# Optimization experiments

Measured on AMD Instinct MI355X. Metric: run time of the kernel, lower is better.

The kernel has to match this reference:

```python
import jax, jax.numpy as jnp
import numpy as np

N, E, IN_DIM, HID, PROJ, NG = 50000, 1600000, 128, 128, 128, 64


def setup_inputs() -> dict:
    key = jax.random.key(0)
    ks = jax.random.split(key, 12)
    def glorot(k, fan_in, fan_out):
        s = (6.0 / (fan_in + fan_out)) ** 0.5
        return jax.random.uniform(k, (fan_in, fan_out), jnp.float32, -s, s)
    x = jax.random.normal(ks[0], (N, IN_DIM), jnp.float32)
    edge_index = jax.random.randint(ks[1], (2, E), 0, N, jnp.int32)
    batch = jnp.sort(jax.random.randint(ks[2], (N,), 0, NG, jnp.int32))
    return {
        "x": x,
        "edge_index": edge_index,
        "batch": batch,
        "num_graphs": NG,
        "W1": glorot(ks[3], IN_DIM, HID), "b1": jnp.zeros((HID,), jnp.float32),
        "W2": glorot(ks[4], HID, HID),    "b2": jnp.zeros((HID,), jnp.float32),
        "pW1": glorot(ks[5], HID, HID),   "pb1": jnp.zeros((HID,), jnp.float32),
        "pW2": glorot(ks[6], HID, PROJ),  "pb2": jnp.zeros((PROJ,), jnp.float32),
    }


def _gcn_norm(edge_index, n_nodes):
    # add self loops, compute symmetric normalization (PyG GCNConv default)
    loop = jnp.arange(n_nodes, dtype=edge_index.dtype)
    src = jnp.concatenate([edge_index[0], loop])
    dst = jnp.concatenate([edge_index[1], loop])
    deg = jax.ops.segment_sum(jnp.ones_like(dst, jnp.float32), dst, num_segments=n_nodes)
    dinv = jnp.where(deg > 0, jax.lax.rsqrt(deg), 0.0)
    norm = dinv[src] * dinv[dst]  # [E+N]
    return src, dst, norm


def _gcn_conv(h, W, b, src, dst, norm, n_nodes):
    hw = h @ W                              # [N, out]
    msg = hw[src] * norm[:, None]           # gather + scale, [E+N, out]
    out = jax.ops.segment_sum(msg, dst, num_segments=n_nodes)  # scatter-add
    return out + b


def reference(x, edge_index, batch, num_graphs, W1, b1, W2, b2, pW1, pb1, pW2, pb2):
    n_nodes = x.shape[0]
    src, dst, norm = _gcn_norm(edge_index, n_nodes)
    # conv stack (dropout is identity in eval mode)
    h = jax.nn.relu(_gcn_conv(x, W1, b1, src, dst, norm, n_nodes))
    h = jax.nn.relu(_gcn_conv(h, W2, b2, src, dst, norm, n_nodes))
    # global mean pool over graphs
    sums = jax.ops.segment_sum(h, batch, num_segments=num_graphs)
    cnts = jax.ops.segment_sum(jnp.ones((n_nodes,), h.dtype), batch, num_segments=num_graphs)
    hg = sums / jnp.maximum(cnts, 1.0)[:, None]
    # MLP projection head
    z = jax.nn.relu(hg @ pW1 + pb1) @ pW2 + pb2
    # L2 normalize (torch F.normalize with eps=1e-12)
    nrm = jnp.maximum(jnp.linalg.norm(z, axis=1, keepdims=True), 1e-12)
    return z / nrm
```

## Files before the change

kernel.cpp:

```cpp
#include <hip/hip_runtime.h>
#include <cstdint>
#include <cstddef>


using short8 = __attribute__((ext_vector_type(8))) short;
using f32x4v = __attribute__((ext_vector_type(4))) float;


static __device__ __forceinline__ unsigned f2bf_rne(float f) {
    unsigned u = __float_as_uint(f);
    return (u + 0x7FFFu + ((u >> 16) & 1u)) >> 16;
}
static __device__ __forceinline__ unsigned pack_bf2(float lo, float hi) {
    return f2bf_rne(lo) | (f2bf_rne(hi) << 16);
}
static __device__ __forceinline__ float bf_lo(unsigned v) {
    return __uint_as_float(v << 16);
}
static __device__ __forceinline__ float bf_hi(unsigned v) {
    return __uint_as_float(v & 0xFFFF0000u);
}


__global__ void k_bincount(const int* __restrict__ dst, int* __restrict__ bcnt,
                           int E, int NB) {
    __shared__ int h[256];
    int t = threadIdx.x;
    h[t] = 0;
    __syncthreads();
    int base_i = blockIdx.x * 4096;
#pragma unroll
    for (int j = 0; j < 16; ++j) {
        int i = base_i + j * 256 + t;
        if (i < E) atomicAdd(&h[dst[i] >> 8], 1);
    }
    __syncthreads();
    if (t < NB && h[t]) atomicAdd(&bcnt[t], h[t]);
}

__global__ void k_bscan(const int* __restrict__ bcnt, int* __restrict__ bbase,
                        int* __restrict__ bcur, int NB) {
    __shared__ int s[256];
    int t = threadIdx.x;
    int v = (t < NB) ? bcnt[t] : 0;
    s[t] = v;
    __syncthreads();
    for (int d = 1; d < 256; d <<= 1) {
        int x = (t >= d) ? s[t - d] : 0;
        __syncthreads();
        s[t] += x;
        __syncthreads();
    }
    if (t < NB) {
        int excl = s[t] - v;
        bbase[t] = excl;
        bcur[t]  = excl;
        if (t == NB - 1) bbase[NB] = s[t];
    }
}


__global__ void k_bin(const int* __restrict__ src, const int* __restrict__ dst,
                      int* __restrict__ bcur, int* __restrict__ bkt,
                      int E, int NB) {
    __shared__ int cnt[256];
    __shared__ int pos[256];
    int t = threadIdx.x;
    int base_i = blockIdx.x * 4096;

    cnt[t] = 0;
    __syncthreads();

    int b_[16];
    int v_[16];
#pragma unroll
    for (int j = 0; j < 16; ++j) {
        int i = base_i + j * 256 + t;
        if (i < E) {
            int s = src[i], d = dst[i];
            v_[j] = s | ((d & 255) << 16);
            int b = d >> 8;
            b_[j] = b;
            atomicAdd(&cnt[b], 1);
        } else {
            b_[j] = -1;
        }
    }
    __syncthreads();

    if (t < NB) {
        int c = cnt[t];
        pos[t] = c ? atomicAdd(&bcur[t], c) : 0;
    }
    __syncthreads();

#pragma unroll
    for (int j = 0; j < 16; ++j) {
        if (b_[j] >= 0) {
            int p = atomicAdd(&pos[b_[j]], 1);
            bkt[p] = v_[j];
        }
    }
}


__global__ void k_fill2(const int* __restrict__ bkt, const int* __restrict__ bbase,
                        int* __restrict__ off, float* __restrict__ dinv,
                        int* __restrict__ csr, int N, int E, int NB) {
    __shared__ int hist[256];
    __shared__ int loff[256];
    __shared__ int cur[256];
    int b = blockIdx.x, t = threadIdx.x;
    if (t < 256) hist[t] = 0;
    __syncthreads();

    int e0 = bbase[b], e1 = bbase[b + 1];
    for (int i = e0 + t; i < e1; i += 1024)
        atomicAdd(&hist[(bkt[i] >> 16) & 255], 1);
    __syncthreads();

    if (t < 256) loff[t] = hist[t];
    __syncthreads();
    for (int d = 1; d < 256; d <<= 1) {
        int x = 0;
        if (t < 256 && t >= d) x = loff[t - d];
        __syncthreads();
        if (t < 256) loff[t] += x;
        __syncthreads();
    }

    if (t < 256) {
        int n = (b << 8) + t;
        if (n < N) {
            int base = e0 + loff[t] - hist[t];
            off[n]  = base;
            cur[t]  = base;
            dinv[n] = rsqrtf((float)(hist[t] + 1));
        }
    }
    if (b == NB - 1 && t == 0) off[N] = E;
    __syncthreads();

    for (int i = e0 + t; i < e1; i += 1024) {
        int v  = bkt[i];
        int dl = (v >> 16) & 255;
        int p  = atomicAdd(&cur[dl], 1);
        csr[p] = v & 0xFFFF;
    }
}


__global__ void k_wprep(const float* __restrict__ Wa, const float* __restrict__ Wb,
                        unsigned short* __restrict__ Ta, unsigned short* __restrict__ Tb) {
    const float* W = blockIdx.x ? Wb : Wa;
    unsigned short* T = blockIdx.x ? Tb : Ta;
    for (int idx = threadIdx.x; idx < 16384; idx += 256) {
        int k = idx >> 7, c = idx & 127;
        T[c * 128 + k] = (unsigned short)f2bf_rne(W[idx]);
    }
}


template<bool BF16IN>
__global__ __launch_bounds__(256) void k_gemm(
        const void* __restrict__ in_, const unsigned short* __restrict__ WT,
        const float* __restrict__ dinv, unsigned* __restrict__ outbf, int N) {
    __shared__ float sC[4][16][132];
    int t = threadIdx.x;
    int w  = t >> 6;
    int l  = t & 63;
    int lo = l & 15;
    int hi = l >> 4;
    int rbase = blockIdx.x * 64 + w * 16;
    int row   = rbase + lo;
    int rowc  = (row < N) ? row : (N - 1);

    short8 a[4];
    if constexpr (BF16IN) {
        const uint4* pu = (const uint4*)in_;
#pragma unroll
        for (int ks = 0; ks < 4; ++ks)
            a[ks] = __builtin_bit_cast(short8, pu[(size_t)rowc * 16 + ks * 4 + hi]);
    } else {
        const float4* pf = (const float4*)in_;
#pragma unroll
        for (int ks = 0; ks < 4; ++ks) {
            float4 fA = pf[(size_t)rowc * 32 + ks * 8 + hi * 2];
            float4 fB = pf[(size_t)rowc * 32 + ks * 8 + hi * 2 + 1];
            short8 s;
            s[0] = (short)f2bf_rne(fA.x); s[1] = (short)f2bf_rne(fA.y);
            s[2] = (short)f2bf_rne(fA.z); s[3] = (short)f2bf_rne(fA.w);
            s[4] = (short)f2bf_rne(fB.x); s[5] = (short)f2bf_rne(fB.y);
            s[6] = (short)f2bf_rne(fB.z); s[7] = (short)f2bf_rne(fB.w);
            a[ks] = s;
        }
    }

    f32x4v acc[8];
#pragma unroll
    for (int i = 0; i < 8; ++i) acc[i] = (f32x4v){0.f, 0.f, 0.f, 0.f};

    const uint4* wt4 = (const uint4*)WT;
#pragma unroll
    for (int cp = 0; cp < 2; ++cp) {
        short8 b[4][4];
#pragma unroll
        for (int ct = 0; ct < 4; ++ct) {
            int col = cp * 64 + ct * 16 + lo;
#pragma unroll
            for (int ks = 0; ks < 4; ++ks)
                b[ct][ks] = __builtin_bit_cast(short8, wt4[col * 16 + ks * 4 + hi]);
        }
#pragma unroll
        for (int ks = 0; ks < 4; ++ks)
#pragma unroll
            for (int ct = 0; ct < 4; ++ct)
                acc[cp * 4 + ct] = __builtin_amdgcn_mfma_f32_16x16x32_bf16(
                    a[ks], b[ct][ks], acc[cp * 4 + ct], 0, 0, 0);
    }

#pragma unroll
    for (int i = 0; i < 8; ++i) {
        int colb = (i >> 2) * 64 + (i & 3) * 16 + lo;
#pragma unroll
        for (int r = 0; r < 4; ++r)
            sC[w][hi * 4 + r][colb] = acc[i][r];
    }
    __syncthreads();

    if (row < N) {
        float d = dinv[rowc];
#pragma unroll
        for (int j = 0; j < 4; ++j) {
            float4 fA = *reinterpret_cast<const float4*>(&sC[w][lo][hi * 32 + j * 8]);
            float4 fB = *reinterpret_cast<const float4*>(&sC[w][lo][hi * 32 + j * 8 + 4]);
            uint4 o = { pack_bf2(fA.x * d, fA.y * d), pack_bf2(fA.z * d, fA.w * d),
                        pack_bf2(fB.x * d, fB.y * d), pack_bf2(fB.z * d, fB.w * d) };
            reinterpret_cast<uint4*>(outbf)[(size_t)row * 16 + hi * 4 + j] = o;
        }
    }
}


__global__ void k_aggr(const unsigned* __restrict__ hw, const int* __restrict__ off,
                       const int* __restrict__ csr, const float* __restrict__ dinv,
                       const float* __restrict__ bias, unsigned* __restrict__ out, int N) {
    int wid  = (blockIdx.x * blockDim.x + threadIdx.x) >> 6;
    int lane = threadIdx.x & 63;
    if (wid >= N) return;
    int n  = wid;
    int q  = lane >> 4;
    int li = lane & 15;

    const uint4* hw4 = reinterpret_cast<const uint4*>(hw);

    float a0 = 0.f, a1 = 0.f, a2 = 0.f, a3 = 0.f;
    float a4 = 0.f, a5 = 0.f, a6 = 0.f, a7 = 0.f;
    if (q == 0) {
        uint4 v = hw4[(unsigned)(n << 4) + li];
        a0 = bf_lo(v.x); a1 = bf_hi(v.x);
        a2 = bf_lo(v.y); a3 = bf_hi(v.y);
        a4 = bf_lo(v.z); a5 = bf_hi(v.z);
        a6 = bf_lo(v.w); a7 = bf_hi(v.w);
    }

    int e = off[n], e1 = off[n + 1];
    while (e < e1) {
        int rem = e1 - e;
        int cnt = rem < 64 ? rem : 64;
        int s_l = N;
        if (lane < cnt) s_l = csr[e + lane];
        int jn = (cnt + 3) >> 2;
#pragma unroll 4
        for (int j = 0; j < jn; ++j) {
            int   s = __shfl(s_l, 4 * j + q);
            uint4 v = hw4[(unsigned)(s << 4) + li];
            a0 += bf_lo(v.x); a1 += bf_hi(v.x);
            a2 += bf_lo(v.y); a3 += bf_hi(v.y);
            a4 += bf_lo(v.z); a5 += bf_hi(v.z);
            a6 += bf_lo(v.w); a7 += bf_hi(v.w);
        }
        e += cnt;
    }

    int p1 = (lane + 32) & 63;
    a0 += __shfl(a0, p1); a1 += __shfl(a1, p1);
    a2 += __shfl(a2, p1); a3 += __shfl(a3, p1);
    a4 += __shfl(a4, p1); a5 += __shfl(a5, p1);
    a6 += __shfl(a6, p1); a7 += __shfl(a7, p1);
    int p2 = (lane + 16) & 63;
    a0 += __shfl(a0, p2); a1 += __shfl(a1, p2);
    a2 += __shfl(a2, p2); a3 += __shfl(a3, p2);
    a4 += __shfl(a4, p2); a5 += __shfl(a5, p2);
    a6 += __shfl(a6, p2); a7 += __shfl(a7, p2);

    if (q == 0) {
        float di = dinv[n];
        const float4* b4 = reinterpret_cast<const float4*>(bias);
        float4 bA = b4[2 * li], bB = b4[2 * li + 1];
        a0 = fmaxf(fmaf(a0, di, bA.x), 0.f); a1 = fmaxf(fmaf(a1, di, bA.y), 0.f);
        a2 = fmaxf(fmaf(a2, di, bA.z), 0.f); a3 = fmaxf(fmaf(a3, di, bA.w), 0.f);
        a4 = fmaxf(fmaf(a4, di, bB.x), 0.f); a5 = fmaxf(fmaf(a5, di, bB.y), 0.f);
        a6 = fmaxf(fmaf(a6, di, bB.z), 0.f); a7 = fmaxf(fmaf(a7, di, bB.w), 0.f);
        uint4 r = { pack_bf2(a0, a1), pack_bf2(a2, a3),
                    pack_bf2(a4, a5), pack_bf2(a6, a7) };
        reinterpret_cast<uint4*>(out)[(unsigned)(n << 4) + li] = r;
    }
}


__global__ void k_pool(const unsigned* __restrict__ h, const int* __restrict__ batch,
                       float* __restrict__ pooled, int* __restrict__ cnt,
                       int N, int npw) {
    int wid  = (blockIdx.x * blockDim.x + threadIdx.x) >> 6;
    int lane = threadIdx.x & 63;
    int n0 = wid * npw;
    if (n0 >= N) return;
    int n1 = n0 + npw; if (n1 > N) n1 = N;

    float ax = 0.f, ay = 0.f;
    int g = batch[n0];
    int c = 0;
    for (int n = n0; n < n1; ++n) {
        int gn = batch[n];
        if (gn != g) {
            atomicAdd(&pooled[g * 128 + 2 * lane],     ax);
            atomicAdd(&pooled[g * 128 + 2 * lane + 1], ay);
            if (lane == 0) atomicAdd(&cnt[g], c);
            ax = 0.f; ay = 0.f; c = 0; g = gn;
        }
        unsigned v = h[(size_t)n * 64 + lane];
        ax += bf_lo(v); ay += bf_hi(v); ++c;
    }
    atomicAdd(&pooled[g * 128 + 2 * lane],     ax);
    atomicAdd(&pooled[g * 128 + 2 * lane + 1], ay);
    if (lane == 0) atomicAdd(&cnt[g], c);
}


__global__ void k_head(const float* __restrict__ pooled, const int* __restrict__ cnt,
                       const float* __restrict__ pW1, const float* __restrict__ pb1,
                       const float* __restrict__ pW2, const float* __restrict__ pb2,
                       float* __restrict__ out) {
    __shared__ float hg[128];
    __shared__ float z1[128];
    __shared__ float red[128];
    int g = blockIdx.x, t = threadIdx.x;

    float c = fmaxf((float)cnt[g], 1.0f);
    hg[t] = pooled[g * 128 + t] / c;
    __syncthreads();

    float a = pb1[t];
#pragma unroll 8
    for (int k = 0; k < 128; ++k) a = fmaf(hg[k], pW1[k * 128 + t], a);
    z1[t] = fmaxf(a, 0.f);
    __syncthreads();

    float z = pb2[t];
#pragma unroll 8
    for (int k = 0; k < 128; ++k) z = fmaf(z1[k], pW2[k * 128 + t], z);

    red[t] = z * z;
    __syncthreads();
    for (int d = 64; d > 0; d >>= 1) {
        if (t < d) red[t] += red[t + d];
        __syncthreads();
    }
    float nrm = fmaxf(sqrtf(red[0]), 1e-12f);
    out[g * 128 + t] = z / nrm;
}


extern "C" void kernel_launch(void* const* d_in, const int* in_sizes, int n_in,
                              void* d_out, int out_size, void* d_ws, size_t ws_size,
                              hipStream_t stream) {
    const float* x    = (const float*)d_in[0];
    const int*   eidx = (const int*)  d_in[1];
    const int*   batch= (const int*)  d_in[2];
    const float* W1   = (const float*)d_in[4];
    const float* b1   = (const float*)d_in[5];
    const float* W2   = (const float*)d_in[6];
    const float* b2   = (const float*)d_in[7];
    const float* pW1  = (const float*)d_in[8];
    const float* pb1  = (const float*)d_in[9];
    const float* pW2  = (const float*)d_in[10];
    const float* pb2  = (const float*)d_in[11];
    float* out = (float*)d_out;

    const int N  = in_sizes[0] / 128;
    const int E  = in_sizes[1] / 2;
    const int NG = out_size / 128;
    const int NB = (N + 255) >> 8;

    const int* src = eidx;
    const int* dst = eidx + E;

    char* p = (char*)d_ws;
    auto alloc = [&](size_t bytes) -> void* {
        void* r = (void*)p;
        p += (bytes + 255) & ~(size_t)255;
        return r;
    };
    int*      bcnt     = (int*)     alloc((size_t)NB * 4);
    int*      bbase    = (int*)     alloc((size_t)(NB + 1) * 4);
    int*      bcur     = (int*)     alloc((size_t)NB * 4);
    int*      off      = (int*)     alloc((size_t)(N + 1) * 4);
    float*    dinv     = (float*)   alloc((size_t)N * 4);
    int*      bkt      = (int*)     alloc((size_t)E * 4);
    int*      csr      = (int*)     alloc((size_t)E * 4);
    unsigned short* wbt1 = (unsigned short*)alloc(16384 * 2);
    unsigned short* wbt2 = (unsigned short*)alloc(16384 * 2);
    unsigned* bufH     = (unsigned*)alloc((size_t)(N + 1) * 64 * 4);
    unsigned* bufB     = (unsigned*)alloc((size_t)N * 64 * 4);
    float*    pooled   = (float*)   alloc((size_t)NG * 128 * 4);
    int*      cnt      = (int*)     alloc((size_t)NG * 4);

    const int tB = (E + 4095) / 4096;

    hipMemsetAsync(bcnt,   0, (size_t)NB * 4, stream);
    hipMemsetAsync(bufH + (size_t)N * 64, 0, 256, stream);
    hipMemsetAsync(pooled, 0, (size_t)NG * 128 * 4, stream);
    hipMemsetAsync(cnt,    0, (size_t)NG * 4, stream);

    k_bincount<<<tB, 256, 0, stream>>>(dst, bcnt, E, NB);
    k_bscan   <<<1, 256, 0, stream>>>(bcnt, bbase, bcur, NB);
    k_bin     <<<tB, 256, 0, stream>>>(src, dst, bcur, bkt, E, NB);
    k_fill2   <<<NB, 1024, 0, stream>>>(bkt, bbase, off, dinv, csr, N, E, NB);
    k_wprep   <<<2, 256, 0, stream>>>(W1, W2, wbt1, wbt2);

    const int gB = (N + 63) / 64;
    const int aB = (N + 3) / 4;

    k_gemm<false><<<gB, 256, 0, stream>>>((const void*)x, wbt1, dinv, bufH, N);
    k_aggr<<<aB, 256, 0, stream>>>(bufH, off, csr, dinv, b1, bufB, N);
    k_gemm<true><<<gB, 256, 0, stream>>>((const void*)bufB, wbt2, dinv, bufH, N);
    k_aggr<<<aB, 256, 0, stream>>>(bufH, off, csr, dinv, b2, bufB, N);

    const int NPW = 32;
    const int waves = (N + NPW - 1) / NPW;
    const int pB = (waves * 64 + 255) / 256;
    k_pool<<<pB, 256, 0, stream>>>(bufB, batch, pooled, cnt, N, NPW);

    k_head<<<NG, 128, 0, stream>>>(pooled, cnt, pW1, pb1, pW2, pb2, out);
}
```

Measured before the change: 262.2 us.

## Fuse weight bf16 transpose into GEMM via LDS and unroll aggregation gathers

Removes the separate k_wprep launch. Each GEMM block now loads the fp32 weight matrix, converts it to bf16, transposes it into padded LDS and reads its B fragments from there instead of from a global pre-transposed buffer. This saves one launch and a dependency, but every one of about 782 blocks now redoes the full weight conversion and adds an extra barrier, and the LDS stores during the transpose may hit bank conflicts. Separately, the aggregation loop is manually unrolled by 8 and then 4, issuing independent gathers ahead of the accumulates so more loads are in flight.

```diff
diff --git a/kernel.cpp b/kernel.cpp
--- a/kernel.cpp
+++ b/kernel.cpp
@@ -150,27 +150,32 @@
 }
 
 
-__global__ void k_wprep(const float* __restrict__ Wa, const float* __restrict__ Wb,
-                        unsigned short* __restrict__ Ta, unsigned short* __restrict__ Tb) {
-    const float* W = blockIdx.x ? Wb : Wa;
-    unsigned short* T = blockIdx.x ? Tb : Ta;
-    for (int idx = threadIdx.x; idx < 16384; idx += 256) {
-        int k = idx >> 7, c = idx & 127;
-        T[c * 128 + k] = (unsigned short)f2bf_rne(W[idx]);
-    }
-}
-
-
 template<bool BF16IN>
 __global__ __launch_bounds__(256) void k_gemm(
-        const void* __restrict__ in_, const unsigned short* __restrict__ WT,
+        const void* __restrict__ in_, const float* __restrict__ W,
         const float* __restrict__ dinv, unsigned* __restrict__ outbf, int N) {
-    __shared__ float sC[4][16][132];
+    __shared__ __align__(16) char smem[34816];
+    unsigned short* wbf = (unsigned short*)smem;
+    float*          sCf = (float*)smem;
+
     int t = threadIdx.x;
     int w  = t >> 6;
     int l  = t & 63;
     int lo = l & 15;
     int hi = l >> 4;
+
+#pragma unroll
+    for (int i = 0; i < 16; ++i) {
+        int idx = (i * 256 + t) * 4;
+        float4 wv = *reinterpret_cast<const float4*>(W + idx);
+        int k = idx >> 7, c = idx & 127;
+        wbf[(c    ) * 136 + k] = (unsigned short)f2bf_rne(wv.x);
+        wbf[(c + 1) * 136 + k] = (unsigned short)f2bf_rne(wv.y);
+        wbf[(c + 2) * 136 + k] = (unsigned short)f2bf_rne(wv.z);
+        wbf[(c + 3) * 136 + k] = (unsigned short)f2bf_rne(wv.w);
+    }
+    __syncthreads();
+
     int rbase = blockIdx.x * 64 + w * 16;
     int row   = rbase + lo;
     int rowc  = (row < N) ? row : (N - 1);
@@ -200,7 +205,6 @@
 #pragma unroll
     for (int i = 0; i < 8; ++i) acc[i] = (f32x4v){0.f, 0.f, 0.f, 0.f};
 
-    const uint4* wt4 = (const uint4*)WT;
 #pragma unroll
     for (int cp = 0; cp < 2; ++cp) {
         short8 b[4][4];
@@ -209,7 +213,8 @@
             int col = cp * 64 + ct * 16 + lo;
 #pragma unroll
             for (int ks = 0; ks < 4; ++ks)
-                b[ct][ks] = __builtin_bit_cast(short8, wt4[col * 16 + ks * 4 + hi]);
+                b[ct][ks] = *reinterpret_cast<const short8*>(
+                    &wbf[col * 136 + ks * 32 + hi * 8]);
         }
 #pragma unroll
         for (int ks = 0; ks < 4; ++ks)
@@ -218,13 +223,14 @@
                 acc[cp * 4 + ct] = __builtin_amdgcn_mfma_f32_16x16x32_bf16(
                     a[ks], b[ct][ks], acc[cp * 4 + ct], 0, 0, 0);
     }
+    __syncthreads();
 
 #pragma unroll
     for (int i = 0; i < 8; ++i) {
         int colb = (i >> 2) * 64 + (i & 3) * 16 + lo;
 #pragma unroll
         for (int r = 0; r < 4; ++r)
-            sC[w][hi * 4 + r][colb] = acc[i][r];
+            sCf[(w * 16 + hi * 4 + r) * 132 + colb] = acc[i][r];
     }
     __syncthreads();
 
@@ -232,8 +238,10 @@
         float d = dinv[rowc];
 #pragma unroll
         for (int j = 0; j < 4; ++j) {
-            float4 fA = *reinterpret_cast<const float4*>(&sC[w][lo][hi * 32 + j * 8]);
-            float4 fB = *reinterpret_cast<const float4*>(&sC[w][lo][hi * 32 + j * 8 + 4]);
+            float4 fA = *reinterpret_cast<const float4*>(
+                &sCf[(w * 16 + lo) * 132 + hi * 32 + j * 8]);
+            float4 fB = *reinterpret_cast<const float4*>(
+                &sCf[(w * 16 + lo) * 132 + hi * 32 + j * 8 + 4]);
             uint4 o = { pack_bf2(fA.x * d, fA.y * d), pack_bf2(fA.z * d, fA.w * d),
                         pack_bf2(fB.x * d, fB.y * d), pack_bf2(fB.z * d, fB.w * d) };
             reinterpret_cast<uint4*>(outbf)[(size_t)row * 16 + hi * 4 + j] = o;
@@ -264,6 +272,12 @@
         a6 = bf_lo(v.w); a7 = bf_hi(v.w);
     }
 
+#define ACC8(v) \
+    a0 += bf_lo(v.x); a1 += bf_hi(v.x); \
+    a2 += bf_lo(v.y); a3 += bf_hi(v.y); \
+    a4 += bf_lo(v.z); a5 += bf_hi(v.z); \
+    a6 += bf_lo(v.w); a7 += bf_hi(v.w);
+
     int e = off[n], e1 = off[n + 1];
     while (e < e1) {
         int rem = e1 - e;
@@ -271,17 +285,46 @@
         int s_l = N;
         if (lane < cnt) s_l = csr[e + lane];
         int jn = (cnt + 3) >> 2;
-#pragma unroll 4
-        for (int j = 0; j < jn; ++j) {
+        int j = 0;
+        for (; j + 8 <= jn; j += 8) {
+            int s0 = __shfl(s_l, 4 * j + q);
+            int s1 = __shfl(s_l, 4 * j + 4 + q);
+            int s2 = __shfl(s_l, 4 * j + 8 + q);
+            int s3 = __shfl(s_l, 4 * j + 12 + q);
+            int s4 = __shfl(s_l, 4 * j + 16 + q);
+            int s5 = __shfl(s_l, 4 * j + 20 + q);
+            int s6 = __shfl(s_l, 4 * j + 24 + q);
+            int s7 = __shfl(s_l, 4 * j + 28 + q);
+            uint4 v0 = hw4[(unsigned)(s0 << 4) + li];
+            uint4 v1 = hw4[(unsigned)(s1 << 4) + li];
+            uint4 v2 = hw4[(unsigned)(s2 << 4) + li];
+            uint4 v3 = hw4[(unsigned)(s3 << 4) + li];
+            uint4 v4 = hw4[(unsigned)(s4 << 4) + li];
+            uint4 v5 = hw4[(unsigned)(s5 << 4) + li];
+            uint4 v6 = hw4[(unsigned)(s6 << 4) + li];
+            uint4 v7 = hw4[(unsigned)(s7 << 4) + li];
+            ACC8(v0) ACC8(v1) ACC8(v2) ACC8(v3)
+            ACC8(v4) ACC8(v5) ACC8(v6) ACC8(v7)
+        }
+        for (; j + 4 <= jn; j += 4) {
+            int s0 = __shfl(s_l, 4 * j + q);
+            int s1 = __shfl(s_l, 4 * j + 4 + q);
+            int s2 = __shfl(s_l, 4 * j + 8 + q);
+            int s3 = __shfl(s_l, 4 * j + 12 + q);
+            uint4 v0 = hw4[(unsigned)(s0 << 4) + li];
+            uint4 v1 = hw4[(unsigned)(s1 << 4) + li];
+            uint4 v2 = hw4[(unsigned)(s2 << 4) + li];
+            uint4 v3 = hw4[(unsigned)(s3 << 4) + li];
+            ACC8(v0) ACC8(v1) ACC8(v2) ACC8(v3)
+        }
+        for (; j < jn; ++j) {
             int   s = __shfl(s_l, 4 * j + q);
             uint4 v = hw4[(unsigned)(s << 4) + li];
-            a0 += bf_lo(v.x); a1 += bf_hi(v.x);
-            a2 += bf_lo(v.y); a3 += bf_hi(v.y);
-            a4 += bf_lo(v.z); a5 += bf_hi(v.z);
-            a6 += bf_lo(v.w); a7 += bf_hi(v.w);
+            ACC8(v)
         }
         e += cnt;
     }
+#undef ACC8
 
     int p1 = (lane + 32) & 63;
     a0 += __shfl(a0, p1); a1 += __shfl(a1, p1);
@@ -409,8 +452,6 @@
     float*    dinv     = (float*)   alloc((size_t)N * 4);
     int*      bkt      = (int*)     alloc((size_t)E * 4);
     int*      csr      = (int*)     alloc((size_t)E * 4);
-    unsigned short* wbt1 = (unsigned short*)alloc(16384 * 2);
-    unsigned short* wbt2 = (unsigned short*)alloc(16384 * 2);
     unsigned* bufH     = (unsigned*)alloc((size_t)(N + 1) * 64 * 4);
     unsigned* bufB     = (unsigned*)alloc((size_t)N * 64 * 4);
     float*    pooled   = (float*)   alloc((size_t)NG * 128 * 4);
@@ -427,14 +468,13 @@
     k_bscan   <<<1, 256, 0, stream>>>(bcnt, bbase, bcur, NB);
     k_bin     <<<tB, 256, 0, stream>>>(src, dst, bcur, bkt, E, NB);
     k_fill2   <<<NB, 1024, 0, stream>>>(bkt, bbase, off, dinv, csr, N, E, NB);
-    k_wprep   <<<2, 256, 0, stream>>>(W1, W2, wbt1, wbt2);
 
     const int gB = (N + 63) / 64;
     const int aB = (N + 3) / 4;
 
-    k_gemm<false><<<gB, 256, 0, stream>>>((const void*)x, wbt1, dinv, bufH, N);
+    k_gemm<false><<<gB, 256, 0, stream>>>((const void*)x, W1, dinv, bufH, N);
     k_aggr<<<aB, 256, 0, stream>>>(bufH, off, csr, dinv, b1, bufB, N);
-    k_gemm<true><<<gB, 256, 0, stream>>>((const void*)bufB, wbt2, dinv, bufH, N);
+    k_gemm<true><<<gB, 256, 0, stream>>>((const void*)bufB, W2, dinv, bufH, N);
     k_aggr<<<aB, 256, 0, stream>>>(bufH, off, csr, dinv, b2, bufB, N);
 
     const int NPW = 32;
```

Result: faster. 237.9 us (-9.3%).
